# Kernel optimization log

Measured on AMD Instinct MI355X. Metric: run time of the kernel, lower is better.

Reference implementation:

```python
import jax, jax.numpy as jnp
import numpy as np

N_NODES = 100000
N_EDGES = 1600000
IN_DIM = 64
F1, F2, F3 = 64, 64, 32
EPS = 1e-12  # torch F.normalize eps


def _glorot(key, shape):
    fan_in, fan_out = shape[0], shape[1]
    lim = (6.0 / (fan_in + fan_out)) ** 0.5
    return jax.random.uniform(key, shape, jnp.float32, -lim, lim)


def setup_inputs() -> dict:
    key = jax.random.key(0)
    ks = jax.random.split(key, 16)
    features_1 = jax.random.normal(ks[0], (N_NODES, IN_DIM), jnp.float32)
    edge_index_1 = jax.random.randint(ks[1], (2, N_EDGES), 0, N_NODES, jnp.int64)
    return {
        "features_1": features_1,
        "edge_index_1": edge_index_1,
        # SAGEConv 1: lin_l (aggregated, with bias), lin_r (root, no bias)
        "W1l": _glorot(ks[2], (IN_DIM, F1)), "b1": jnp.zeros((F1,), jnp.float32), "W1r": _glorot(ks[3], (IN_DIM, F1)),
        "W2l": _glorot(ks[4], (F1, F2)), "b2": jnp.zeros((F2,), jnp.float32), "W2r": _glorot(ks[5], (F1, F2)),
        "W3l": _glorot(ks[6], (F2, F3)), "b3": jnp.zeros((F3,), jnp.float32), "W3r": _glorot(ks[7], (F2, F3)),
        # SimGNN attention pooling weight [F3, F3]
        "W_att": _glorot(ks[8], (F3, F3)),
        # MLP head
        "W_fc": _glorot(ks[9], (F3, 16)), "b_fc": jnp.zeros((16,), jnp.float32),
        "W_s": _glorot(ks[10], (16, 1)), "b_s": jnp.zeros((1,), jnp.float32),
    }


def _sage_conv(x, src, tgt, Wl, b, Wr):
    # mean-aggregate source features at target nodes (PyG SAGEConv, aggr='mean')
    msg_sum = jax.ops.segment_sum(x[src], tgt, num_segments=N_NODES)  # [N, F]
    deg = jax.ops.segment_sum(jnp.ones((src.shape[0],), x.dtype), tgt, num_segments=N_NODES)
    agg = msg_sum / jnp.maximum(deg, 1.0)[:, None]
    out = agg @ Wl + b + x @ Wr
    # normalize=True -> L2 normalize per node
    norm = jnp.linalg.norm(out, axis=-1, keepdims=True)
    return out / jnp.maximum(norm, EPS)


def reference(features_1, edge_index_1, W1l, b1, W1r, W2l, b2, W2r, W3l, b3, W3r, W_att, W_fc, b_fc, W_s, b_s):
    src, tgt = edge_index_1[0], edge_index_1[1]
    h = _sage_conv(features_1, src, tgt, W1l, b1, W1r)
    h = jax.nn.relu(h)  # dropout p=0 / eval mode -> identity
    h = _sage_conv(h, src, tgt, W2l, b2, W2r)
    h = jax.nn.relu(h)
    h = _sage_conv(h, src, tgt, W3l, b3, W3r)  # [N, F3]
    # SimGNN attention pooling
    context = jnp.tanh(jnp.mean(h @ W_att, axis=0))          # [F3]
    att = jax.nn.sigmoid(h @ context)                         # [N]
    pooled = (att @ h)[None, :]                               # [1, F3]
    hidden = jax.nn.relu(pooled @ W_fc + b_fc)                # [1, 16]
    score = jax.nn.sigmoid(hidden @ W_s + b_s)                # [1, 1]
    return score
```

## Files before the change

### kernel.cpp

```cpp
#include <hip/hip_runtime.h>
#include <hip/hip_bf16.h>
#include <hip/hip_fp16.h>
#include <math.h>

#define N_NODES 100000
#define N_EDGES 1600000
#define SCAN_BLOCKS 98
#define XCD_RANGE 12500

typedef _Float16 h8 __attribute__((ext_vector_type(8)));
typedef float f32x4 __attribute__((ext_vector_type(4)));

__device__ __forceinline__ float bcast(float v, int l) {
    return __int_as_float(__builtin_amdgcn_readlane(__float_as_int(v), l));
}

__global__ __launch_bounds__(256) void k_cvt(const float* __restrict__ in,
                                             _Float16* __restrict__ out) {
    int i = blockIdx.x * 256 + threadIdx.x;
    const f32x4* p = reinterpret_cast<const f32x4*>(in) + (size_t)i * 2;
    f32x4 u = __builtin_nontemporal_load(p);
    f32x4 v = __builtin_nontemporal_load(p + 1);
    h8 o;
    o[0] = u[0]; o[1] = u[1]; o[2] = u[2]; o[3] = u[3];
    o[4] = v[0]; o[5] = v[1]; o[6] = v[2]; o[7] = v[3];
    *(reinterpret_cast<h8*>(out) + i) = o;
}

__global__ __launch_bounds__(256) void k_count(const int* __restrict__ tgt,
                                               int* __restrict__ counts) {
    int p = blockIdx.x & 7;
    int e = (blockIdx.x >> 3) * 256 + threadIdx.x;
    int t = __builtin_nontemporal_load(tgt + e);
    if ((unsigned)(t - p * XCD_RANGE) < XCD_RANGE) atomicAdd(&counts[t], 1);
}

__global__ __launch_bounds__(256) void k_scanA(const int* __restrict__ counts,
                                               int* __restrict__ rowptr,
                                               int* __restrict__ bsum) {
    int t = threadIdx.x;
    int base = blockIdx.x * 1024 + t * 4;
    int v0 = (base + 0 < N_NODES) ? counts[base + 0] : 0;
    int v1 = (base + 1 < N_NODES) ? counts[base + 1] : 0;
    int v2 = (base + 2 < N_NODES) ? counts[base + 2] : 0;
    int v3 = (base + 3 < N_NODES) ? counts[base + 3] : 0;
    int s = v0 + v1 + v2 + v3;
    __shared__ int sS[256];
    sS[t] = s;
    __syncthreads();
    for (int off = 1; off < 256; off <<= 1) {
        int add = (t >= off) ? sS[t - off] : 0;
        __syncthreads();
        sS[t] += add;
        __syncthreads();
    }
    int excl = sS[t] - s;
    if (t == 255) bsum[blockIdx.x] = sS[255];
    if (base + 0 < N_NODES) rowptr[base + 0] = excl;
    if (base + 1 < N_NODES) rowptr[base + 1] = excl + v0;
    if (base + 2 < N_NODES) rowptr[base + 2] = excl + v0 + v1;
    if (base + 3 < N_NODES) rowptr[base + 3] = excl + v0 + v1 + v2;
}

__global__ void k_scanB(const int* __restrict__ bsum, int* __restrict__ boff) {
    __shared__ int sD[128];
    int t = threadIdx.x;
    int v = (t < SCAN_BLOCKS) ? bsum[t] : 0;
    sD[t] = v;
    __syncthreads();
    for (int off = 1; off < 128; off <<= 1) {
        int add = (t >= off) ? sD[t - off] : 0;
        __syncthreads();
        sD[t] += add;
        __syncthreads();
    }
    boff[t] = sD[t] - v;
}

__global__ __launch_bounds__(256) void k_scanC(int* __restrict__ rowptr,
                                               const int* __restrict__ boff) {
    int t = threadIdx.x;
    int base = blockIdx.x * 1024 + t * 4;
    int add = boff[blockIdx.x];
    if (base + 0 < N_NODES) rowptr[base + 0] += add;
    if (base + 1 < N_NODES) rowptr[base + 1] += add;
    if (base + 2 < N_NODES) rowptr[base + 2] += add;
    if (base + 3 < N_NODES) rowptr[base + 3] += add;
}

__global__ __launch_bounds__(256) void k_fill(const int* __restrict__ ei,
                                              int* __restrict__ rowptr,
                                              int* __restrict__ csr) {
    int p = blockIdx.x & 7;
    int e = (blockIdx.x >> 3) * 256 + threadIdx.x;
    int t = __builtin_nontemporal_load(ei + N_EDGES + e);
    if ((unsigned)(t - p * XCD_RANGE) < XCD_RANGE) {
        int s = __builtin_nontemporal_load(ei + e);
        int pos = atomicAdd(&rowptr[t], 1);
        csr[pos] = s;
    }
}

template <int LD>
__device__ __forceinline__ void gadd(float (&A)[8], const _Float16* __restrict__ x,
                                     int idx, int n, int cnt, int c8) {
    int s = __shfl(idx, n);
    h8 v = *reinterpret_cast<const h8*>(x + (size_t)s * LD + c8);
    float m = (n < cnt) ? 1.0f : 0.0f;
#pragma unroll
    for (int j = 0; j < 8; ++j) A[j] = fmaf((float)v[j], m, A[j]);
}

__global__ __launch_bounds__(256) void k_gather64(const _Float16* __restrict__ x,
                                                  const int* __restrict__ rowptr,
                                                  const int* __restrict__ csr,
                                                  _Float16* __restrict__ agg) {
    int wid = (blockIdx.x * 256 + threadIdx.x) >> 6;
    int lane = threadIdx.x & 63;
    if (wid >= N_NODES) return;
    int rs = (wid > 0) ? rowptr[wid - 1] : 0;
    int re = rowptr[wid];
    int sub = lane >> 3;
    int c8 = (lane & 7) * 8;
    float a0[8] = {0}, a1[8] = {0}, a2[8] = {0}, a3[8] = {0};
    for (int base = rs; base < re; base += 64) {
        int j = base + lane;
        int idx = (j < re) ? csr[j] : 0;
        int cnt = min(64, re - base);
        {
            gadd<64>(a0, x, idx, 0 + sub, cnt, c8);
            gadd<64>(a1, x, idx, 8 + sub, cnt, c8);
        }
        if (16 < cnt) {
            gadd<64>(a2, x, idx, 16 + sub, cnt, c8);
            gadd<64>(a3, x, idx, 24 + sub, cnt, c8);
        }
        if (32 < cnt) {
            gadd<64>(a0, x, idx, 32 + sub, cnt, c8);
            gadd<64>(a1, x, idx, 40 + sub, cnt, c8);
        }
        if (48 < cnt) {
            gadd<64>(a2, x, idx, 48 + sub, cnt, c8);
            gadd<64>(a3, x, idx, 56 + sub, cnt, c8);
        }
    }
    float acc[8];
#pragma unroll
    for (int j = 0; j < 8; ++j) acc[j] = (a0[j] + a1[j]) + (a2[j] + a3[j]);
#pragma unroll
    for (int m = 8; m <= 32; m <<= 1) {
#pragma unroll
        for (int j = 0; j < 8; ++j) acc[j] += __shfl_xor(acc[j], m);
    }
    if (lane < 8) {
        float invd = 1.0f / fmaxf((float)(re - rs), 1.0f);
        h8 o;
#pragma unroll
        for (int j = 0; j < 8; ++j) o[j] = (_Float16)(acc[j] * invd);
        *reinterpret_cast<h8*>(agg + (size_t)wid * 64 + c8) = o;
    }
}

template <bool RELU>
__global__ __launch_bounds__(256) void k_xform64m(const _Float16* __restrict__ x,
                                                  const _Float16* __restrict__ agg,
                                                  const float* __restrict__ Wl,
                                                  const float* __restrict__ b,
                                                  const float* __restrict__ Wr,
                                                  _Float16* __restrict__ out) {
    int lane = threadIdx.x & 63;
    int g = lane >> 4;
    int r = lane & 15;
    int wv = (blockIdx.x * 256 + threadIdx.x) >> 6;
    int nw = gridDim.x * 4;
    h8 wl[2][4], wr[2][4];
#pragma unroll
    for (int kt = 0; kt < 2; ++kt)
#pragma unroll
        for (int ct = 0; ct < 4; ++ct)
#pragma unroll
            for (int j = 0; j < 8; ++j) {
                int row = kt * 32 + g * 8 + j, col = ct * 16 + r;
                wl[kt][ct][j] = (_Float16)Wl[row * 64 + col];
                wr[kt][ct][j] = (_Float16)Wr[row * 64 + col];
            }
    float biasv[4];
#pragma unroll
    for (int ct = 0; ct < 4; ++ct) biasv[ct] = b[ct * 16 + r];
    for (int tile = wv; tile < N_NODES / 16; tile += nw) {
        int n0 = tile * 16;
        const h8* arow = reinterpret_cast<const h8*>(agg + (size_t)(n0 + r) * 64);
        const h8* xrow = reinterpret_cast<const h8*>(x + (size_t)(n0 + r) * 64);
        h8 aa0 = arow[g], aa1 = arow[4 + g];
        h8 ax0 = xrow[g], ax1 = xrow[4 + g];
        f32x4 acc[4];
#pragma unroll
        for (int ct = 0; ct < 4; ++ct) {
            acc[ct] = (f32x4){biasv[ct], biasv[ct], biasv[ct], biasv[ct]};
            acc[ct] = __builtin_amdgcn_mfma_f32_16x16x32_f16(aa0, wl[0][ct], acc[ct], 0, 0, 0);
            acc[ct] = __builtin_amdgcn_mfma_f32_16x16x32_f16(aa1, wl[1][ct], acc[ct], 0, 0, 0);
            acc[ct] = __builtin_amdgcn_mfma_f32_16x16x32_f16(ax0, wr[0][ct], acc[ct], 0, 0, 0);
            acc[ct] = __builtin_amdgcn_mfma_f32_16x16x32_f16(ax1, wr[1][ct], acc[ct], 0, 0, 0);
        }
#pragma unroll
        for (int reg = 0; reg < 4; ++reg) {
            float ss = acc[0][reg] * acc[0][reg] + acc[1][reg] * acc[1][reg] +
                       acc[2][reg] * acc[2][reg] + acc[3][reg] * acc[3][reg];
            ss += __shfl_xor(ss, 1);
            ss += __shfl_xor(ss, 2);
            ss += __shfl_xor(ss, 4);
            ss += __shfl_xor(ss, 8);
            float rinv = 1.0f / fmaxf(sqrtf(ss), 1e-12f);
            int row = n0 + g * 4 + reg;
#pragma unroll
            for (int ct = 0; ct < 4; ++ct) {
                float v = acc[ct][reg] * rinv;
                if (RELU) v = fmaxf(v, 0.0f);
                out[(size_t)row * 64 + ct * 16 + r] = (_Float16)v;
            }
        }
    }
}

__global__ __launch_bounds__(256) void k_xform64z(const _Float16* __restrict__ x,
                                                  const _Float16* __restrict__ agg,
                                                  const float* __restrict__ Wl,
                                                  const float* __restrict__ b,
                                                  const float* __restrict__ Wr,
                                                  const float* __restrict__ W3l,
                                                  const float* __restrict__ W3r,
                                                  _Float16* __restrict__ z,
                                                  _Float16* __restrict__ r3) {
    int lane = threadIdx.x & 63;
    int g = lane >> 4;
    int r = lane & 15;
    int wv4 = threadIdx.x >> 6;
    int wv = (blockIdx.x * 256 + threadIdx.x) >> 6;
    int nw = gridDim.x * 4;
    __shared__ _Float16 sT[4][16][72];
    h8 wl[2][4], wr[2][4];
#pragma unroll
    for (int kt = 0; kt < 2; ++kt)
#pragma unroll
        for (int ct = 0; ct < 4; ++ct)
#pragma unroll
            for (int j = 0; j < 8; ++j) {
                int row = kt * 32 + g * 8 + j, col = ct * 16 + r;
                wl[kt][ct][j] = (_Float16)Wl[row * 64 + col];
                wr[kt][ct][j] = (_Float16)Wr[row * 64 + col];
            }
    h8 wz[2][2], w3[2][2];
#pragma unroll
    for (int kt = 0; kt < 2; ++kt)
#pragma unroll
        for (int ct = 0; ct < 2; ++ct)
#pragma unroll
            for (int j = 0; j < 8; ++j) {
                int row = kt * 32 + g * 8 + j, col = ct * 16 + r;
                wz[kt][ct][j] = (_Float16)W3l[row * 32 + col];
                w3[kt][ct][j] = (_Float16)W3r[row * 32 + col];
            }
    float biasv[4];
#pragma unroll
    for (int ct = 0; ct < 4; ++ct) biasv[ct] = b[ct * 16 + r];
    for (int tile = wv; tile < N_NODES / 16; tile += nw) {
        int n0 = tile * 16;
        const h8* arow = reinterpret_cast<const h8*>(agg + (size_t)(n0 + r) * 64);
        const h8* xrow = reinterpret_cast<const h8*>(x + (size_t)(n0 + r) * 64);
        h8 aa0 = arow[g], aa1 = arow[4 + g];
        h8 ax0 = xrow[g], ax1 = xrow[4 + g];
        f32x4 acc[4];
#pragma unroll
        for (int ct = 0; ct < 4; ++ct) {
            acc[ct] = (f32x4){biasv[ct], biasv[ct], biasv[ct], biasv[ct]};
            acc[ct] = __builtin_amdgcn_mfma_f32_16x16x32_f16(aa0, wl[0][ct], acc[ct], 0, 0, 0);
            acc[ct] = __builtin_amdgcn_mfma_f32_16x16x32_f16(aa1, wl[1][ct], acc[ct], 0, 0, 0);
            acc[ct] = __builtin_amdgcn_mfma_f32_16x16x32_f16(ax0, wr[0][ct], acc[ct], 0, 0, 0);
            acc[ct] = __builtin_amdgcn_mfma_f32_16x16x32_f16(ax1, wr[1][ct], acc[ct], 0, 0, 0);
        }
#pragma unroll
        for (int reg = 0; reg < 4; ++reg) {
            float ss = acc[0][reg] * acc[0][reg] + acc[1][reg] * acc[1][reg] +
                       acc[2][reg] * acc[2][reg] + acc[3][reg] * acc[3][reg];
            ss += __shfl_xor(ss, 1);
            ss += __shfl_xor(ss, 2);
            ss += __shfl_xor(ss, 4);
            ss += __shfl_xor(ss, 8);
            float rinv = 1.0f / fmaxf(sqrtf(ss), 1e-12f);
            int row16 = g * 4 + reg;
#pragma unroll
            for (int ct = 0; ct < 4; ++ct) {
                float v = fmaxf(acc[ct][reg] * rinv, 0.0f);
                sT[wv4][row16][ct * 16 + r] = (_Float16)v;
            }
        }
        h8 ha0 = *reinterpret_cast<const h8*>(&sT[wv4][r][g * 8]);
        h8 ha1 = *reinterpret_cast<const h8*>(&sT[wv4][r][32 + g * 8]);
        f32x4 zacc[2], racc[2];
#pragma unroll
        for (int ct = 0; ct < 2; ++ct) {
            zacc[ct] = (f32x4){0, 0, 0, 0};
            zacc[ct] = __builtin_amdgcn_mfma_f32_16x16x32_f16(ha0, wz[0][ct], zacc[ct], 0, 0, 0);
            zacc[ct] = __builtin_amdgcn_mfma_f32_16x16x32_f16(ha1, wz[1][ct], zacc[ct], 0, 0, 0);
            racc[ct] = (f32x4){0, 0, 0, 0};
            racc[ct] = __builtin_amdgcn_mfma_f32_16x16x32_f16(ha0, w3[0][ct], racc[ct], 0, 0, 0);
            racc[ct] = __builtin_amdgcn_mfma_f32_16x16x32_f16(ha1, w3[1][ct], racc[ct], 0, 0, 0);
        }
#pragma unroll
        for (int reg = 0; reg < 4; ++reg) {
            int row = n0 + g * 4 + reg;
#pragma unroll
            for (int ct = 0; ct < 2; ++ct) {
                z[(size_t)row * 32 + ct * 16 + r] = (_Float16)zacc[ct][reg];
                r3[(size_t)row * 32 + ct * 16 + r] = (_Float16)racc[ct][reg];
            }
        }
    }
}

__global__ __launch_bounds__(256) void k_g32fin(const _Float16* __restrict__ z,
                                                const int* __restrict__ rowptr,
                                                const int* __restrict__ csr,
                                                const _Float16* __restrict__ r3,
                                                const float* __restrict__ b3,
                                                float* __restrict__ h3) {
    int wid = (blockIdx.x * 256 + threadIdx.x) >> 6;
    int lane = threadIdx.x & 63;
    if (wid >= N_NODES) return;
    int sub = lane >> 2;
    int c8 = (lane & 3) * 8;
    float bb[8];
#pragma unroll
    for (int j = 0; j < 8; ++j) bb[j] = b3[c8 + j];
    int rs = (wid > 0) ? rowptr[wid - 1] : 0;
    int re = rowptr[wid];
    float a0[8] = {0}, a1[8] = {0}, a2[8] = {0}, a3[8] = {0};
    for (int base = rs; base < re; base += 64) {
        int j = base + lane;
        int idx = (j < re) ? csr[j] : 0;
        int cnt = min(64, re - base);
        gadd<32>(a0, z, idx, 0 + sub, cnt, c8);
        if (16 < cnt) gadd<32>(a1, z, idx, 16 + sub, cnt, c8);
        if (32 < cnt) gadd<32>(a2, z, idx, 32 + sub, cnt, c8);
        if (48 < cnt) gadd<32>(a3, z, idx, 48 + sub, cnt, c8);
    }
    float acc[8];
#pragma unroll
    for (int j = 0; j < 8; ++j) acc[j] = (a0[j] + a1[j]) + (a2[j] + a3[j]);
#pragma unroll
    for (int m = 4; m <= 32; m <<= 1) {
#pragma unroll
        for (int j = 0; j < 8; ++j) acc[j] += __shfl_xor(acc[j], m);
    }
    float invd = 1.0f / fmaxf((float)(re - rs), 1.0f);
    h8 rr = (lane < 4) ? *reinterpret_cast<const h8*>(r3 + (size_t)wid * 32 + c8)
                       : (h8){0, 0, 0, 0, 0, 0, 0, 0};
    float val[8];
    float ss = 0.f;
#pragma unroll
    for (int j = 0; j < 8; ++j) {
        val[j] = fmaf(acc[j], invd, (float)rr[j] + bb[j]);
        ss = fmaf(val[j], val[j], ss);
    }
    ss += __shfl_xor(ss, 1);
    ss += __shfl_xor(ss, 2);
    if (lane < 4) {
        float rinv = 1.0f / fmaxf(sqrtf(ss), 1e-12f);
        f32x4 o0 = {val[0] * rinv, val[1] * rinv, val[2] * rinv, val[3] * rinv};
        f32x4 o1 = {val[4] * rinv, val[5] * rinv, val[6] * rinv, val[7] * rinv};
        f32x4* op = reinterpret_cast<f32x4*>(h3 + (size_t)wid * 32 + c8);
        op[0] = o0;
        op[1] = o1;
    }
}

__global__ __launch_bounds__(256) void k_colsum(const float* __restrict__ h,
                                                float* __restrict__ colsum) {
    int gid = blockIdx.x * 256 + threadIdx.x;
    const int total = N_NODES * 32;
    const int stride = 1024 * 256;
    float s = 0.0f;
    for (int i = gid; i < total; i += stride) s += h[i];
    s += __shfl_xor(s, 32);
    __shared__ float sP[4][32];
    int wave = threadIdx.x >> 6, lane = threadIdx.x & 63;
    if (lane < 32) sP[wave][lane] = s;
    __syncthreads();
    if (threadIdx.x < 32) {
        float v = sP[0][threadIdx.x] + sP[1][threadIdx.x] + sP[2][threadIdx.x] +
                  sP[3][threadIdx.x];
        atomicAdd(&colsum[threadIdx.x], v);
    }
}

__global__ __launch_bounds__(256) void k_attpool(const float* __restrict__ h,
                                                 const float* __restrict__ colsum,
                                                 const float* __restrict__ Watt,
                                                 float* __restrict__ pooled) {
    __shared__ float sC[32];
    __shared__ float sP[4][32];
    int t = threadIdx.x;
    if (t < 32) {
        float acc = 0.0f;
#pragma unroll
        for (int f = 0; f < 32; ++f)
            acc += (colsum[f] * (1.0f / N_NODES)) * Watt[f * 32 + t];
        sC[t] = tanhf(acc);
    }
    __syncthreads();
    float p[32];
#pragma unroll
    for (int f = 0; f < 32; ++f) p[f] = 0.f;
    int stride = gridDim.x * 256;
    for (int n = blockIdx.x * 256 + t; n < N_NODES; n += stride) {
        const f32x4* row = reinterpret_cast<const f32x4*>(h + (size_t)n * 32);
        f32x4 r[8];
        float dot = 0.0f;
#pragma unroll
        for (int q = 0; q < 8; ++q) {
            r[q] = row[q];
            dot += r[q][0] * sC[q * 4] + r[q][1] * sC[q * 4 + 1] +
                   r[q][2] * sC[q * 4 + 2] + r[q][3] * sC[q * 4 + 3];
        }
        float att = 1.0f / (1.0f + expf(-dot));
#pragma unroll
        for (int q = 0; q < 8; ++q) {
            p[q * 4 + 0] = fmaf(att, r[q][0], p[q * 4 + 0]);
            p[q * 4 + 1] = fmaf(att, r[q][1], p[q * 4 + 1]);
            p[q * 4 + 2] = fmaf(att, r[q][2], p[q * 4 + 2]);
            p[q * 4 + 3] = fmaf(att, r[q][3], p[q * 4 + 3]);
        }
    }
#pragma unroll
    for (int f = 0; f < 32; ++f) {
#pragma unroll
        for (int m = 1; m < 64; m <<= 1) p[f] += __shfl_xor(p[f], m);
    }
    int wave = t >> 6, lane = t & 63;
    if (lane == 0) {
#pragma unroll
        for (int f = 0; f < 32; ++f) sP[wave][f] = p[f];
    }
    __syncthreads();
    if (t < 32) {
        float v = sP[0][t] + sP[1][t] + sP[2][t] + sP[3][t];
        atomicAdd(&pooled[t], v);
    }
}

__global__ void k_head(const float* __restrict__ pooled,
                       const float* __restrict__ Wfc, const float* __restrict__ bfc,
                       const float* __restrict__ Ws, const float* __restrict__ bs,
                       float* __restrict__ out) {
    __shared__ float sH[16];
    int t = threadIdx.x;
    if (t < 16) {
        float acc = bfc[t];
#pragma unroll
        for (int f = 0; f < 32; ++f) acc += pooled[f] * Wfc[f * 16 + t];
        sH[t] = fmaxf(acc, 0.0f);
    }
    __syncthreads();
    if (t == 0) {
        float s = bs[0];
#pragma unroll
        for (int j = 0; j < 16; ++j) s += sH[j] * Ws[j];
        out[0] = 1.0f / (1.0f + expf(-s));
    }
}

extern "C" void kernel_launch(void* const* d_in, const int* in_sizes, int n_in,
                              void* d_out, int out_size, void* d_ws, size_t ws_size,
                              hipStream_t stream) {
    const float* feat = (const float*)d_in[0];
    const int* ei = (const int*)d_in[1];
    const float* W1l = (const float*)d_in[2];
    const float* b1 = (const float*)d_in[3];
    const float* W1r = (const float*)d_in[4];
    const float* W2l = (const float*)d_in[5];
    const float* b2 = (const float*)d_in[6];
    const float* W2r = (const float*)d_in[7];
    const float* W3l = (const float*)d_in[8];
    const float* b3 = (const float*)d_in[9];
    const float* W3r = (const float*)d_in[10];
    const float* Watt = (const float*)d_in[11];
    const float* Wfc = (const float*)d_in[12];
    const float* bfc = (const float*)d_in[13];
    const float* Ws = (const float*)d_in[14];
    const float* bs = (const float*)d_in[15];
    float* out = (float*)d_out;

    int* rowptr = (int*)d_ws;
    int* bsum = rowptr + 100000;
    int* boff = bsum + 128;
    int* counts = boff + 128;
    int* csr = counts + 100000;
    _Float16* B1 = (_Float16*)(csr + N_EDGES);
    _Float16* B2 = B1 + (size_t)N_NODES * 64;
    _Float16* B3 = B2 + (size_t)N_NODES * 64;
    float* h3 = (float*)(B3 + (size_t)N_NODES * 64);
    float* colsum = h3 + (size_t)N_NODES * 32;
    float* pooled = colsum + 32;

    hipMemsetAsync(counts, 0, N_NODES * sizeof(int), stream);
    hipMemsetAsync(colsum, 0, 64 * sizeof(float), stream);
    k_cvt<<<3125, 256, 0, stream>>>(feat, B1);
    k_count<<<(N_EDGES / 256) * 8, 256, 0, stream>>>(ei + N_EDGES, counts);
    k_scanA<<<SCAN_BLOCKS, 256, 0, stream>>>(counts, rowptr, bsum);
    k_scanB<<<1, 128, 0, stream>>>(bsum, boff);
    k_scanC<<<SCAN_BLOCKS, 256, 0, stream>>>(rowptr, boff);
    k_fill<<<(N_EDGES / 256) * 8, 256, 0, stream>>>(ei, rowptr, csr);

    k_gather64<<<25000, 256, 0, stream>>>(B1, rowptr, csr, B2);
    k_xform64m<true><<<512, 256, 0, stream>>>(B1, B2, W1l, b1, W1r, B3);

    _Float16* z = B1;
    _Float16* r3 = B1 + (size_t)N_NODES * 32;
    k_gather64<<<25000, 256, 0, stream>>>(B3, rowptr, csr, B2);
    k_xform64z<<<512, 256, 0, stream>>>(B3, B2, W2l, b2, W2r, W3l, W3r, z, r3);

    k_g32fin<<<25000, 256, 0, stream>>>(z, rowptr, csr, r3, b3, h3);

    k_colsum<<<1024, 256, 0, stream>>>(h3, colsum);
    k_attpool<<<391, 256, 0, stream>>>(h3, colsum, Watt, pooled);
    k_head<<<1, 64, 0, stream>>>(pooled, Wfc, bfc, Ws, bs, out);
}
```

Baseline: 464.0 us.

## Fuse preprocessing kernels, single-pass decoupled scan, and fold head into attpool

Merges the fp16 conversion and degree counting into one launch, and drops the XCD-partitioned counting in favour of plain atomics over all edges. Replaces the three-kernel scan with one kernel that chains block offsets through flag spin-waits. Moves the MLP head into the last block of the attention-pooling kernel using a done counter. The aim is to cut launch count and the extra passes. The risks are more global atomic contention on counts and a serial lookback whose spin-waits rely on earlier blocks having been scheduled.

```diff
diff --git a/kernel.cpp b/kernel.cpp
--- a/kernel.cpp
+++ b/kernel.cpp
@@ -7,39 +7,39 @@
 #define N_EDGES 1600000
 #define SCAN_BLOCKS 98
 #define XCD_RANGE 12500
+#define CVT_BLOCKS 3125
+#define CNT_BLOCKS 6250
+#define ATT_BLOCKS 391
 
 typedef _Float16 h8 __attribute__((ext_vector_type(8)));
 typedef float f32x4 __attribute__((ext_vector_type(4)));
 
-__device__ __forceinline__ float bcast(float v, int l) {
-    return __int_as_float(__builtin_amdgcn_readlane(__float_as_int(v), l));
-}
-
-__global__ __launch_bounds__(256) void k_cvt(const float* __restrict__ in,
-                                             _Float16* __restrict__ out) {
-    int i = blockIdx.x * 256 + threadIdx.x;
-    const f32x4* p = reinterpret_cast<const f32x4*>(in) + (size_t)i * 2;
-    f32x4 u = __builtin_nontemporal_load(p);
-    f32x4 v = __builtin_nontemporal_load(p + 1);
-    h8 o;
-    o[0] = u[0]; o[1] = u[1]; o[2] = u[2]; o[3] = u[3];
-    o[4] = v[0]; o[5] = v[1]; o[6] = v[2]; o[7] = v[3];
-    *(reinterpret_cast<h8*>(out) + i) = o;
-}
-
-__global__ __launch_bounds__(256) void k_count(const int* __restrict__ tgt,
-                                               int* __restrict__ counts) {
-    int p = blockIdx.x & 7;
-    int e = (blockIdx.x >> 3) * 256 + threadIdx.x;
-    int t = __builtin_nontemporal_load(tgt + e);
-    if ((unsigned)(t - p * XCD_RANGE) < XCD_RANGE) atomicAdd(&counts[t], 1);
-}
-
-__global__ __launch_bounds__(256) void k_scanA(const int* __restrict__ counts,
-                                               int* __restrict__ rowptr,
-                                               int* __restrict__ bsum) {
-    int t = threadIdx.x;
-    int base = blockIdx.x * 1024 + t * 4;
+__global__ __launch_bounds__(256) void k_cvtcount(const float* __restrict__ feat,
+                                                  _Float16* __restrict__ outH,
+                                                  const int* __restrict__ tgt,
+                                                  int* __restrict__ counts) {
+    int b = blockIdx.x, t = threadIdx.x;
+    if (b < CVT_BLOCKS) {
+        int i = b * 256 + t;
+        const f32x4* p = reinterpret_cast<const f32x4*>(feat) + (size_t)i * 2;
+        f32x4 u = __builtin_nontemporal_load(p);
+        f32x4 v = __builtin_nontemporal_load(p + 1);
+        h8 o;
+        o[0] = u[0]; o[1] = u[1]; o[2] = u[2]; o[3] = u[3];
+        o[4] = v[0]; o[5] = v[1]; o[6] = v[2]; o[7] = v[3];
+        *(reinterpret_cast<h8*>(outH) + i) = o;
+    } else {
+        int e = (b - CVT_BLOCKS) * 256 + t;
+        atomicAdd(&counts[__builtin_nontemporal_load(tgt + e)], 1);
+    }
+}
+
+__global__ __launch_bounds__(256) void k_scan(const int* __restrict__ counts,
+                                              int* __restrict__ rowptr,
+                                              int* __restrict__ agg,
+                                              int* __restrict__ flag) {
+    int b = blockIdx.x, t = threadIdx.x;
+    int base = b * 1024 + t * 4;
     int v0 = (base + 0 < N_NODES) ? counts[base + 0] : 0;
     int v1 = (base + 1 < N_NODES) ? counts[base + 1] : 0;
     int v2 = (base + 2 < N_NODES) ? counts[base + 2] : 0;
@@ -55,37 +55,26 @@
         __syncthreads();
     }
     int excl = sS[t] - s;
-    if (t == 255) bsum[blockIdx.x] = sS[255];
-    if (base + 0 < N_NODES) rowptr[base + 0] = excl;
-    if (base + 1 < N_NODES) rowptr[base + 1] = excl + v0;
-    if (base + 2 < N_NODES) rowptr[base + 2] = excl + v0 + v1;
-    if (base + 3 < N_NODES) rowptr[base + 3] = excl + v0 + v1 + v2;
-}
-
-__global__ void k_scanB(const int* __restrict__ bsum, int* __restrict__ boff) {
-    __shared__ int sD[128];
-    int t = threadIdx.x;
-    int v = (t < SCAN_BLOCKS) ? bsum[t] : 0;
-    sD[t] = v;
+    if (t == 255) {
+        agg[b] = sS[255];
+        __threadfence();
+        atomicExch(&flag[b], 1);
+    }
+    __shared__ int sOff;
+    if (t == 0) {
+        int off = 0;
+        for (int p = b - 1; p >= 0; --p) {
+            while (atomicAdd(&flag[p], 0) == 0) {}
+            off += atomicAdd(&agg[p], 0);
+        }
+        sOff = off;
+    }
     __syncthreads();
-    for (int off = 1; off < 128; off <<= 1) {
-        int add = (t >= off) ? sD[t - off] : 0;
-        __syncthreads();
-        sD[t] += add;
-        __syncthreads();
-    }
-    boff[t] = sD[t] - v;
-}
-
-__global__ __launch_bounds__(256) void k_scanC(int* __restrict__ rowptr,
-                                               const int* __restrict__ boff) {
-    int t = threadIdx.x;
-    int base = blockIdx.x * 1024 + t * 4;
-    int add = boff[blockIdx.x];
-    if (base + 0 < N_NODES) rowptr[base + 0] += add;
-    if (base + 1 < N_NODES) rowptr[base + 1] += add;
-    if (base + 2 < N_NODES) rowptr[base + 2] += add;
-    if (base + 3 < N_NODES) rowptr[base + 3] += add;
+    int add = sOff;
+    if (base + 0 < N_NODES) rowptr[base + 0] = excl + add;
+    if (base + 1 < N_NODES) rowptr[base + 1] = excl + v0 + add;
+    if (base + 2 < N_NODES) rowptr[base + 2] = excl + v0 + v1 + add;
+    if (base + 3 < N_NODES) rowptr[base + 3] = excl + v0 + v1 + v2 + add;
 }
 
 __global__ __launch_bounds__(256) void k_fill(const int* __restrict__ ei,
@@ -396,7 +385,13 @@
 __global__ __launch_bounds__(256) void k_attpool(const float* __restrict__ h,
                                                  const float* __restrict__ colsum,
                                                  const float* __restrict__ Watt,
-                                                 float* __restrict__ pooled) {
+                                                 float* __restrict__ pooled,
+                                                 int* __restrict__ done,
+                                                 const float* __restrict__ Wfc,
+                                                 const float* __restrict__ bfc,
+                                                 const float* __restrict__ Ws,
+                                                 const float* __restrict__ bs,
+                                                 float* __restrict__ out) {
     __shared__ float sC[32];
     __shared__ float sP[4][32];
     int t = threadIdx.x;
@@ -446,26 +441,28 @@
         float v = sP[0][t] + sP[1][t] + sP[2][t] + sP[3][t];
         atomicAdd(&pooled[t], v);
     }
-}
-
-__global__ void k_head(const float* __restrict__ pooled,
-                       const float* __restrict__ Wfc, const float* __restrict__ bfc,
-                       const float* __restrict__ Ws, const float* __restrict__ bs,
-                       float* __restrict__ out) {
-    __shared__ float sH[16];
-    int t = threadIdx.x;
-    if (t < 16) {
-        float acc = bfc[t];
-#pragma unroll
-        for (int f = 0; f < 32; ++f) acc += pooled[f] * Wfc[f * 16 + t];
-        sH[t] = fmaxf(acc, 0.0f);
-    }
+    __threadfence();
+    __shared__ int sLast;
+    if (t == 0) sLast = atomicAdd(done, 1);
     __syncthreads();
-    if (t == 0) {
-        float s = bs[0];
-#pragma unroll
-        for (int j = 0; j < 16; ++j) s += sH[j] * Ws[j];
-        out[0] = 1.0f / (1.0f + expf(-s));
+    if (sLast == (int)gridDim.x - 1) {
+        __shared__ float sPo[32];
+        __shared__ float sH[16];
+        if (t < 32) sPo[t] = atomicAdd(&pooled[t], 0.0f);
+        __syncthreads();
+        if (t < 16) {
+            float acc = bfc[t];
+#pragma unroll
+            for (int f = 0; f < 32; ++f) acc += sPo[f] * Wfc[f * 16 + t];
+            sH[t] = fmaxf(acc, 0.0f);
+        }
+        __syncthreads();
+        if (t == 0) {
+            float s = bs[0];
+#pragma unroll
+            for (int j = 0; j < 16; ++j) s += sH[j] * Ws[j];
+            out[0] = 1.0f / (1.0f + expf(-s));
+        }
     }
 }
 
@@ -491,24 +488,23 @@
     float* out = (float*)d_out;
 
     int* rowptr = (int*)d_ws;
-    int* bsum = rowptr + 100000;
-    int* boff = bsum + 128;
-    int* counts = boff + 128;
-    int* csr = counts + 100000;
+    int* counts = rowptr + 100000;
+    float* colsum = (float*)(counts + 100000);
+    float* pooled = colsum + 32;
+    int* done = (int*)(pooled + 32);
+    int* flag = done + 4;
+    int* agg = flag + 98;
+    int* csr = agg + 102;
     _Float16* B1 = (_Float16*)(csr + N_EDGES);
     _Float16* B2 = B1 + (size_t)N_NODES * 64;
     _Float16* B3 = B2 + (size_t)N_NODES * 64;
     float* h3 = (float*)(B3 + (size_t)N_NODES * 64);
-    float* colsum = h3 + (size_t)N_NODES * 32;
-    float* pooled = colsum + 32;
 
     hipMemsetAsync(counts, 0, N_NODES * sizeof(int), stream);
-    hipMemsetAsync(colsum, 0, 64 * sizeof(float), stream);
-    k_cvt<<<3125, 256, 0, stream>>>(feat, B1);
-    k_count<<<(N_EDGES / 256) * 8, 256, 0, stream>>>(ei + N_EDGES, counts);
-    k_scanA<<<SCAN_BLOCKS, 256, 0, stream>>>(counts, rowptr, bsum);
-    k_scanB<<<1, 128, 0, stream>>>(bsum, boff);
-    k_scanC<<<SCAN_BLOCKS, 256, 0, stream>>>(rowptr, boff);
+    hipMemsetAsync(colsum, 0, (32 + 32 + 4 + 98) * sizeof(int), stream);
+
+    k_cvtcount<<<CVT_BLOCKS + CNT_BLOCKS, 256, 0, stream>>>(feat, B1, ei + N_EDGES, counts);
+    k_scan<<<SCAN_BLOCKS, 256, 0, stream>>>(counts, rowptr, agg, flag);
     k_fill<<<(N_EDGES / 256) * 8, 256, 0, stream>>>(ei, rowptr, csr);
 
     k_gather64<<<25000, 256, 0, stream>>>(B1, rowptr, csr, B2);
@@ -522,6 +518,6 @@
     k_g32fin<<<25000, 256, 0, stream>>>(z, rowptr, csr, r3, b3, h3);
 
     k_colsum<<<1024, 256, 0, stream>>>(h3, colsum);
-    k_attpool<<<391, 256, 0, stream>>>(h3, colsum, Watt, pooled);
-    k_head<<<1, 64, 0, stream>>>(pooled, Wfc, bfc, Ws, bs, out);
-}
+    k_attpool<<<ATT_BLOCKS, 256, 0, stream>>>(h3, colsum, Watt, pooled, done,
+                                              Wfc, bfc, Ws, bs, out);
+}
```

Result: slower. 515.2 us (+11.0%).
